# Kernel tuning notes

Measured on AMD Instinct MI355X. Metric: run time of the kernel, lower is better.

Reference implementation:

```python
import jax, jax.numpy as jnp
import numpy as np

B, K, D = 131072, 256, 16


def setup_inputs() -> dict:
    key = jax.random.key(0)
    k1, k2 = jax.random.split(key)
    trajectory = jax.random.normal(k1, (B, D), dtype=jnp.float32)
    centers = jax.random.normal(k2, (K, D), dtype=jnp.float32)
    return {"trajectory": trajectory, "centers": centers}


def reference(trajectory, centers):
    # dists[b, k] = ||centers[k] - trajectory[b]||_2 ; argmin over k.
    # Computed via the expanded squared distance to avoid materializing the
    # [B, K, D] broadcast difference tensor (same argmin as torch's norm).
    x2 = jnp.sum(trajectory * trajectory, axis=-1, keepdims=True)      # [B, 1]
    c2 = jnp.sum(centers * centers, axis=-1)                            # [K]
    xc = jnp.einsum('bd,kd->bk', trajectory, centers)                   # [B, K]
    d2 = x2 - 2.0 * xc + c2[None, :]                                    # [B, K]
    center_idxs = jnp.argmin(d2, axis=1)                                # [B]
    offset = trajectory - centers[center_idxs]                          # [B, D]
    return center_idxs, offset
```

## Files before the change

kernel.cpp:

```cpp
#include <hip/hip_runtime.h>


constexpr int Bn = 131072;
constexpr int Kn = 256;
constexpr int Dn = 16;
constexpr int PTS = 128;
constexpr int NW = 4;
constexpr int KC = Kn / NW;

typedef float v2f __attribute__((ext_vector_type(2)));

__global__ __launch_bounds__(256) void prep_kernel(
    const float* __restrict__ centers, float* __restrict__ n2c,
    float* __restrict__ c2) {
  int t = blockIdx.x * 256 + threadIdx.x;
  if (t < Kn * Dn) n2c[t] = -2.0f * centers[t];
  if (t < Kn) {
    const float* c = centers + t * Dn;
    float s = 0.0f;
#pragma unroll
    for (int d = 0; d < Dn; ++d) s = fmaf(c[d], c[d], s);
    c2[t] = s;
  }
}

__global__ __launch_bounds__(256, 8) void kmeans_kernel(
    const float* __restrict__ traj, const float* __restrict__ centers,
    const float* __restrict__ n2c, const float* __restrict__ c2,
    float* __restrict__ out) {
  __shared__ float sbest[NW * PTS];
  __shared__ int sbi[NW * PTS];
  __shared__ int swin[PTS];

  const int t = threadIdx.x;
  const int blk = blockIdx.x;
  const int w = __builtin_amdgcn_readfirstlane(t >> 6);
  const int l = t & 63;
  const int p0 = blk * PTS + l;
  const int p1 = p0 + 64;

  v2f y[Dn];
  {
    const float4* xa = reinterpret_cast<const float4*>(traj + (size_t)p0 * Dn);
    const float4* xb = reinterpret_cast<const float4*>(traj + (size_t)p1 * Dn);
#pragma unroll
    for (int q = 0; q < 4; ++q) {
      float4 a = xa[q], b = xb[q];
      y[q * 4 + 0] = (v2f){a.x, b.x};
      y[q * 4 + 1] = (v2f){a.y, b.y};
      y[q * 4 + 2] = (v2f){a.z, b.z};
      y[q * 4 + 3] = (v2f){a.w, b.w};
    }
  }

  float best0 = __builtin_inff(), best1 = __builtin_inff();
  int bi0 = 0, bi1 = 0;
  const int k0 = w * KC;
#pragma unroll 4
  for (int kk = 0; kk < KC; ++kk) {
    const int k = k0 + kk;
    const float* cr = n2c + k * Dn;
    const float c2k = c2[k];
    v2f acc = (v2f){c2k, c2k};
#pragma unroll
    for (int d = 0; d < Dn; ++d) {
      const float c = cr[d];
      acc = y[d] * (v2f){c, c} + acc;
    }
    if (acc.x < best0) { best0 = acc.x; bi0 = k; }
    if (acc.y < best1) { best1 = acc.y; bi1 = k; }
  }
  sbest[w * PTS + l] = best0;
  sbi[w * PTS + l] = bi0;
  sbest[w * PTS + 64 + l] = best1;
  sbi[w * PTS + 64 + l] = bi1;
  __syncthreads();

  if (t < PTS) {
    float b0 = sbest[t];
    int i0 = sbi[t];
#pragma unroll
    for (int ww = 1; ww < NW; ++ww) {
      float b1 = sbest[ww * PTS + t];
      int i1 = sbi[ww * PTS + t];
      if (b1 < b0) { b0 = b1; i0 = i1; }
    }
    swin[t] = i0;
    out[blk * PTS + t] = (float)i0;
  }
  __syncthreads();

#pragma unroll
  for (int it = 0; it < 2; ++it) {
    const int id = it * 256 + t;
    const int pb = id >> 2, q = id & 3;
    const int pt = blk * PTS + pb;
    const int win = swin[pb];
    float4 xv = reinterpret_cast<const float4*>(traj + (size_t)pt * Dn)[q];
    float4 cv = reinterpret_cast<const float4*>(centers + (size_t)win * Dn)[q];
    float4 o = make_float4(xv.x - cv.x, xv.y - cv.y, xv.z - cv.z, xv.w - cv.w);
    reinterpret_cast<float4*>(out + Bn)[(size_t)pt * 4 + q] = o;
  }
}

extern "C" void kernel_launch(void* const* d_in, const int* in_sizes, int n_in,
                              void* d_out, int out_size, void* d_ws, size_t ws_size,
                              hipStream_t stream) {
  (void)in_sizes; (void)n_in; (void)out_size; (void)ws_size;
  const float* traj = (const float*)d_in[0];
  const float* centers = (const float*)d_in[1];
  float* out = (float*)d_out;

  float* n2c = (float*)d_ws;
  float* c2 = n2c + Kn * Dn;

  prep_kernel<<<16, 256, 0, stream>>>(centers, n2c, c2);
  kmeans_kernel<<<Bn / PTS, 256, 0, stream>>>(traj, centers, n2c, c2, out);
}
```

Baseline: 75.15 us.

## Process four points per lane with pre-duplicated center table and 8 waves

Result: slower. 77.81 us (+3.5%).

```diff
diff --git a/kernel.cpp b/kernel.cpp
--- a/kernel.cpp
+++ b/kernel.cpp
@@ -4,30 +4,37 @@
 constexpr int Bn = 131072;
 constexpr int Kn = 256;
 constexpr int Dn = 16;
-constexpr int PTS = 128;
-constexpr int NW = 4;
+constexpr int PPL = 4;
+constexpr int PTS = PPL * 64;
+constexpr int NW = 8;
 constexpr int KC = Kn / NW;
+constexpr int ROW = 2 + 2 * Dn;
 
 typedef float v2f __attribute__((ext_vector_type(2)));
 
-__global__ __launch_bounds__(256) void prep_kernel(
-    const float* __restrict__ centers, float* __restrict__ n2c,
-    float* __restrict__ c2) {
-  int t = blockIdx.x * 256 + threadIdx.x;
-  if (t < Kn * Dn) n2c[t] = -2.0f * centers[t];
+__global__ __launch_bounds__(64) void prep_kernel(
+    const float* __restrict__ centers, float* __restrict__ tab) {
+  int t = blockIdx.x * 64 + threadIdx.x;
   if (t < Kn) {
     const float* c = centers + t * Dn;
+    float2 buf[17];
     float s = 0.0f;
 #pragma unroll
-    for (int d = 0; d < Dn; ++d) s = fmaf(c[d], c[d], s);
-    c2[t] = s;
+    for (int d = 0; d < Dn; ++d) {
+      float cd = c[d];
+      s = fmaf(cd, cd, s);
+      buf[1 + d] = make_float2(-2.0f * cd, -2.0f * cd);
+    }
+    buf[0] = make_float2(s, s);
+    float2* r = reinterpret_cast<float2*>(tab + (size_t)t * ROW);
+#pragma unroll
+    for (int j = 0; j < 17; ++j) r[j] = buf[j];
   }
 }
 
-__global__ __launch_bounds__(256, 8) void kmeans_kernel(
+__global__ __launch_bounds__(512, 4) void kmeans_kernel(
     const float* __restrict__ traj, const float* __restrict__ centers,
-    const float* __restrict__ n2c, const float* __restrict__ c2,
-    float* __restrict__ out) {
+    const float* __restrict__ tab, float* __restrict__ out) {
   __shared__ float sbest[NW * PTS];
   __shared__ int sbi[NW * PTS];
   __shared__ int swin[PTS];
@@ -36,44 +43,49 @@
   const int blk = blockIdx.x;
   const int w = __builtin_amdgcn_readfirstlane(t >> 6);
   const int l = t & 63;
-  const int p0 = blk * PTS + l;
-  const int p1 = p0 + 64;
+  const int pbase = blk * PTS + l;
 
-  v2f y[Dn];
+  v2f y0[Dn], y1[Dn];
   {
-    const float4* xa = reinterpret_cast<const float4*>(traj + (size_t)p0 * Dn);
-    const float4* xb = reinterpret_cast<const float4*>(traj + (size_t)p1 * Dn);
+    const float4* xa = reinterpret_cast<const float4*>(traj + (size_t)(pbase      ) * Dn);
+    const float4* xb = reinterpret_cast<const float4*>(traj + (size_t)(pbase +  64) * Dn);
+    const float4* xc = reinterpret_cast<const float4*>(traj + (size_t)(pbase + 128) * Dn);
+    const float4* xd = reinterpret_cast<const float4*>(traj + (size_t)(pbase + 192) * Dn);
 #pragma unroll
     for (int q = 0; q < 4; ++q) {
-      float4 a = xa[q], b = xb[q];
-      y[q * 4 + 0] = (v2f){a.x, b.x};
-      y[q * 4 + 1] = (v2f){a.y, b.y};
-      y[q * 4 + 2] = (v2f){a.z, b.z};
-      y[q * 4 + 3] = (v2f){a.w, b.w};
+      float4 a = xa[q], b = xb[q], c = xc[q], d = xd[q];
+      y0[q * 4 + 0] = (v2f){a.x, b.x};  y1[q * 4 + 0] = (v2f){c.x, d.x};
+      y0[q * 4 + 1] = (v2f){a.y, b.y};  y1[q * 4 + 1] = (v2f){c.y, d.y};
+      y0[q * 4 + 2] = (v2f){a.z, b.z};  y1[q * 4 + 2] = (v2f){c.z, d.z};
+      y0[q * 4 + 3] = (v2f){a.w, b.w};  y1[q * 4 + 3] = (v2f){c.w, d.w};
     }
   }
 
   float best0 = __builtin_inff(), best1 = __builtin_inff();
-  int bi0 = 0, bi1 = 0;
+  float best2 = __builtin_inff(), best3 = __builtin_inff();
+  int bi0 = 0, bi1 = 0, bi2 = 0, bi3 = 0;
   const int k0 = w * KC;
-#pragma unroll 4
+#pragma unroll 2
   for (int kk = 0; kk < KC; ++kk) {
     const int k = k0 + kk;
-    const float* cr = n2c + k * Dn;
-    const float c2k = c2[k];
-    v2f acc = (v2f){c2k, c2k};
+    const v2f* row = reinterpret_cast<const v2f*>(tab + (size_t)k * ROW);
+    v2f a0 = row[0];
+    v2f a1 = a0;
 #pragma unroll
     for (int d = 0; d < Dn; ++d) {
-      const float c = cr[d];
-      acc = y[d] * (v2f){c, c} + acc;
+      const v2f c = row[1 + d];
+      a0 = y0[d] * c + a0;
+      a1 = y1[d] * c + a1;
     }
-    if (acc.x < best0) { best0 = acc.x; bi0 = k; }
-    if (acc.y < best1) { best1 = acc.y; bi1 = k; }
+    if (a0.x < best0) { best0 = a0.x; bi0 = k; }
+    if (a0.y < best1) { best1 = a0.y; bi1 = k; }
+    if (a1.x < best2) { best2 = a1.x; bi2 = k; }
+    if (a1.y < best3) { best3 = a1.y; bi3 = k; }
   }
-  sbest[w * PTS + l] = best0;
-  sbi[w * PTS + l] = bi0;
-  sbest[w * PTS + 64 + l] = best1;
-  sbi[w * PTS + 64 + l] = bi1;
+  sbest[w * PTS + l      ] = best0;  sbi[w * PTS + l      ] = bi0;
+  sbest[w * PTS + l +  64] = best1;  sbi[w * PTS + l +  64] = bi1;
+  sbest[w * PTS + l + 128] = best2;  sbi[w * PTS + l + 128] = bi2;
+  sbest[w * PTS + l + 192] = best3;  sbi[w * PTS + l + 192] = bi3;
   __syncthreads();
 
   if (t < PTS) {
@@ -92,7 +104,7 @@
 
 #pragma unroll
   for (int it = 0; it < 2; ++it) {
-    const int id = it * 256 + t;
+    const int id = it * 512 + t;
     const int pb = id >> 2, q = id & 3;
     const int pt = blk * PTS + pb;
     const int win = swin[pb];
@@ -111,9 +123,8 @@
   const float* centers = (const float*)d_in[1];
   float* out = (float*)d_out;
 
-  float* n2c = (float*)d_ws;
-  float* c2 = n2c + Kn * Dn;
+  float* tab = (float*)d_ws;
 
-  prep_kernel<<<16, 256, 0, stream>>>(centers, n2c, c2);
-  kmeans_kernel<<<Bn / PTS, 256, 0, stream>>>(traj, centers, n2c, c2, out);
+  prep_kernel<<<4, 64, 0, stream>>>(centers, tab);
+  kmeans_kernel<<<Bn / PTS, 512, 0, stream>>>(traj, centers, tab, out);
 }
```
